# Kernel optimization log

Hardware: AMD Instinct MI355X
Metric: run time of the kernel (lower is better)

Reference implementation:

```python
import jax, jax.numpy as jnp
import numpy as np

MKT_COEF = jnp.array([0.5, -1.0, 0.8, 0.6, 1.5, 0.4], dtype=jnp.float32)
RISK_COEF = jnp.array([0.5, -0.8, 0.6, 1.0, 1.2, 0.5], dtype=jnp.float32)
PI = 3.14159


def setup_inputs() -> dict:
    key = jax.random.key(0)
    k1, k2, k3, k4 = jax.random.split(key, 4)
    B, S, H, D = 128, 8192, 16, 6
    return {
        "sequence_embeddings": jax.random.normal(k1, (B, S, H), dtype=jnp.float32),
        "market_volatility": jax.random.uniform(k2, (B, S), dtype=jnp.float32),
        "risk_factors": jax.random.normal(k3, (B, S, D), dtype=jnp.float32),
        "router_w": jax.random.normal(k4, (D, H), dtype=jnp.float32) * 0.02,
        "router_b": jnp.zeros((D,), dtype=jnp.float32),
    }


def _expert_predictions(x, assignments):
    # x: (B,S,H); assignments: (B,S) int32
    mean = x.mean(-1, keepdims=True)                       # (B,S,1)
    std = jnp.std(x, axis=-1, keepdims=True, ddof=1)       # torch.std is unbiased
    d0 = jnp.tanh(x[:, :, :4].mean(-1, keepdims=True)) * (1.0 + std)
    d1 = jax.nn.sigmoid(mean) * 0.3 - 0.15
    d2 = x[:, :, :6].mean(-1, keepdims=True) * 0.8 + jnp.sin(x[:, :, 6:10].mean(-1, keepdims=True) * PI) * 0.4
    noise = jax.random.normal(jax.random.key(42), mean.shape, dtype=x.dtype) * 0.05
    d3 = jnp.tanh(x[:, :, :8].mean(-1, keepdims=True)) * 0.9 + noise
    d4 = jax.nn.relu(mean) ** 1.2 + std * 2.5 - 0.5
    d5 = jax.nn.sigmoid(mean) * 0.4 + jnp.tanh(std) * 0.2
    preds_all = jnp.concatenate([d0, d1, d2, d3, d4, d5], axis=-1)  # (B,S,6)
    return jnp.take_along_axis(preds_all, assignments[..., None].astype(jnp.int32), axis=-1)  # (B,S,1)


def reference(sequence_embeddings, market_volatility, risk_factors, router_w, router_b):
    x = sequence_embeddings
    logits = jnp.einsum("bsh,dh->bsd", x, router_w) + router_b            # (B,S,6)
    probs_base = jax.nn.softmax(logits, axis=-1)
    assignments = jnp.argmax(probs_base, axis=-1).astype(jnp.int32)       # (B,S)
    # training-mode market/risk adjusted straight-through probs
    adj = logits + market_volatility[..., None] * MKT_COEF * 0.3 + risk_factors * RISK_COEF * 0.3
    probs_diff = jax.nn.softmax(adj / 1.2, axis=-1)
    routing_probs = jax.lax.stop_gradient(probs_base) + probs_diff - jax.lax.stop_gradient(probs_diff)
    predictions = _expert_predictions(x, assignments)                     # (B,S,1)
    return predictions, routing_probs, assignments
```

## Files before the change

kernel.cpp:

```cpp
#include <hip/hip_runtime.h>
#include <math.h>

typedef float float4v __attribute__((ext_vector_type(4)));
typedef float float2v __attribute__((ext_vector_type(2)));

__device__ __forceinline__ unsigned rotl32(unsigned v, int n) {
  return (v << n) | (v >> (32 - n));
}

__device__ __forceinline__ float frcp(float x) { return __builtin_amdgcn_rcpf(x); }

__device__ __forceinline__ float ftanh(float x) {
  float t = __expf(2.0f * x);
  return 1.0f - 2.0f * frcp(t + 1.0f);
}

__device__ __forceinline__ float fsigmoid(float x) {
  return frcp(1.0f + __expf(-x));
}

__device__ __forceinline__ float jax_threefry_normal42_part(unsigned idx) {
  const unsigned ks0 = 0u;
  const unsigned ks1 = 42u;
  const unsigned ks2 = 0x1BD11BDAu ^ 42u;
  unsigned x0 = 0u + ks0;
  unsigned x1 = idx + ks1;
  const unsigned ks[3] = {ks0, ks1, ks2};
  const int rA[4] = {13, 15, 26, 6};
  const int rB[4] = {17, 29, 16, 24};
#pragma unroll
  for (int i = 0; i < 5; ++i) {
    const int* r = (i & 1) ? rB : rA;
#pragma unroll
    for (int k = 0; k < 4; ++k) {
      x0 += x1;
      x1 = rotl32(x1, r[k]);
      x1 ^= x0;
    }
    x0 += ks[(i + 1) % 3];
    x1 += ks[(i + 2) % 3] + (unsigned)(i + 1);
  }
  unsigned bits = x0 ^ x1;
  float u01 = __uint_as_float((bits >> 9) | 0x3f800000u) - 1.0f;
  const float lo = -0.99999994f;
  float u = fmaxf(lo, fmaf(u01, 2.0f, lo));
  float w = -__logf(1.0f - u * u);
  float p;
  if (w < 5.0f) {
    w = w - 2.5f;
    p = 2.81022636e-08f;
    p = fmaf(p, w, 3.43273939e-07f);
    p = fmaf(p, w, -3.5233877e-06f);
    p = fmaf(p, w, -4.39150654e-06f);
    p = fmaf(p, w, 0.00021858087f);
    p = fmaf(p, w, -0.00125372503f);
    p = fmaf(p, w, -0.00417768164f);
    p = fmaf(p, w, 0.246640727f);
    p = fmaf(p, w, 1.50140941f);
  } else {
    w = sqrtf(w) - 3.0f;
    p = -0.000200214257f;
    p = fmaf(p, w, 0.000100950558f);
    p = fmaf(p, w, 0.00134934322f);
    p = fmaf(p, w, -0.00367342844f);
    p = fmaf(p, w, 0.00573950773f);
    p = fmaf(p, w, -0.0076224613f);
    p = fmaf(p, w, 0.00943887047f);
    p = fmaf(p, w, 1.00167406f);
    p = fmaf(p, w, 2.83297682f);
  }
  return 1.41421354f * (p * u);
}

__device__ __forceinline__ void token_body(
    const float4v a[4], int t, float noise,
    const float* __restrict__ rw, const float* __restrict__ rb,
    float* __restrict__ out, int ntok) {
  float2v x2[8];
  x2[0] = a[0].xy; x2[1] = a[0].zw;
  x2[2] = a[1].xy; x2[3] = a[1].zw;
  x2[4] = a[2].xy; x2[5] = a[2].zw;
  x2[6] = a[3].xy; x2[7] = a[3].zw;
  float x[16];
#pragma unroll
  for (int q = 0; q < 4; ++q) {
    x[q * 4 + 0] = a[q].x; x[q * 4 + 1] = a[q].y;
    x[q * 4 + 2] = a[q].z; x[q * 4 + 3] = a[q].w;
  }

  const float2v* rw2 = reinterpret_cast<const float2v*>(rw);
  float lg[6];
#pragma unroll
  for (int d = 0; d < 6; ++d) {
    float2v acc2; acc2.x = 0.0f; acc2.y = 0.0f;
#pragma unroll
    for (int p = 0; p < 8; ++p)
      acc2 = __builtin_elementwise_fma(x2[p], rw2[d * 8 + p], acc2);
    lg[d] = (acc2.x + acc2.y) + rb[d];
  }

  int a1i = 0, a2i = 0;
  float b1 = lg[0], b2 = -1e30f;
#pragma unroll
  for (int d = 1; d < 6; ++d) {
    if (lg[d] > b1) { b2 = b1; a2i = a1i; b1 = lg[d]; a1i = d; }
    else if (lg[d] > b2) { b2 = lg[d]; a2i = d; }
  }
  int amax = a1i;
  if (b1 - b2 < 2e-5f) {
    double A = 0.0, B = 0.0;
#pragma unroll
    for (int h = 0; h < 16; ++h) {
      A = fma((double)x[h], (double)rw[a1i * 16 + h], A);
      B = fma((double)x[h], (double)rw[a2i * 16 + h], B);
    }
    A += (double)rb[a1i];
    B += (double)rb[a2i];
    amax = (B > A || (B == A && a2i < a1i)) ? a2i : a1i;
  }

  float m = lg[0];
#pragma unroll
  for (int d = 1; d < 6; ++d) m = fmaxf(m, lg[d]);
  float eb[6], se = 0.0f;
#pragma unroll
  for (int d = 0; d < 6; ++d) { eb[d] = __expf(lg[d] - m); se += eb[d]; }
  float inv_se = frcp(se);
  float pb[6];
#pragma unroll
  for (int d = 0; d < 6; ++d) pb[d] = eb[d] * inv_se;

  float2v s2; s2.x = 0.0f; s2.y = 0.0f;
#pragma unroll
  for (int p = 0; p < 8; ++p) s2 = s2 + x2[p];
  float mean = (s2.x + s2.y) * (1.0f / 16.0f);
  float2v mean2; mean2.x = mean; mean2.y = mean;
  float2v ss2; ss2.x = 0.0f; ss2.y = 0.0f;
#pragma unroll
  for (int p = 0; p < 8; ++p) {
    float2v dv = x2[p] - mean2;
    ss2 = __builtin_elementwise_fma(dv, dv, ss2);
  }
  float stdv = sqrtf((ss2.x + ss2.y) * (1.0f / 15.0f));

  float s4 = ((x[0] + x[1]) + x[2]) + x[3];
  float s6 = ((((x[0] + x[1]) + x[2]) + x[3]) + x[4]) + x[5];
  float s610 = ((x[6] + x[7]) + x[8]) + x[9];
  float s8 = s6 + x[6] + x[7];

  float sig = fsigmoid(mean);
  float p0 = ftanh(s4 * 0.25f) * (1.0f + stdv);
  float p1 = sig * 0.3f - 0.15f;
  float p2 = (s6 * (1.0f / 6.0f)) * 0.8f + __sinf((s610 * 0.25f) * 3.14159f) * 0.4f;
  float p3 = ftanh(s8 * 0.125f) * 0.9f + noise;
  float r4 = fmaxf(mean, 0.0f);
  float p4 = __expf(1.2f * __logf(r4)) + stdv * 2.5f - 0.5f;
  float p5 = sig * 0.4f + ftanh(stdv) * 0.2f;

  float pred = (amax == 0) ? p0
             : (amax == 1) ? p1
             : (amax == 2) ? p2
             : (amax == 3) ? p3
             : (amax == 4) ? p4
                           : p5;

  out[t] = pred;
  float2v* po = reinterpret_cast<float2v*>(out + ntok) + (size_t)t * 3;
  float2v v0; v0.x = pb[0]; v0.y = pb[1];
  float2v v1; v1.x = pb[2]; v1.y = pb[3];
  float2v v2; v2.x = pb[4]; v2.y = pb[5];
  po[0] = v0;
  po[1] = v1;
  po[2] = v2;
  out[(size_t)ntok * 7 + t] = (float)amax;
}

__global__ __launch_bounds__(256) void finance_moe_kernel(
    const float* __restrict__ emb,
    const float* __restrict__ rw,
    const float* __restrict__ rb,
    float* __restrict__ out,
    int ntok) {
  __shared__ float lds[256 * 16];

  int tl = threadIdx.x;
  int t = blockIdx.x * 256 + tl;
  bool full = ((blockIdx.x + 1) * 256 <= ntok);

  if (full) {
    int lane = tl & 63;
    int wave = tl >> 6;
    const float* gbase = emb + (size_t)blockIdx.x * 256 * 16;
#pragma unroll
    for (int c = 0; c < 4; ++c) {
      int chunk = wave * 4 + c;
      int slot = chunk * 64 + lane;
      int tok = slot >> 2;
      int s = slot & 3;
      int e = s ^ ((tok >> 1) & 3);
      int gidx = tok * 4 + e;
      const float* gp = gbase + (size_t)gidx * 4;
      __builtin_amdgcn_global_load_lds(
          (const __attribute__((address_space(1))) void*)gp,
          (__attribute__((address_space(3))) void*)(lds + (size_t)chunk * 256),
          16, 0, 0);
    }

    float noise = jax_threefry_normal42_part((unsigned)t) * 0.05f;

    __syncthreads();

    float4v a[4];
#pragma unroll
    for (int q = 0; q < 4; ++q) {
      int s = q ^ ((tl >> 1) & 3);
      a[q] = *reinterpret_cast<const float4v*>(&lds[tl * 16 + s * 4]);
    }

    token_body(a, t, noise, rw, rb, out, ntok);
  } else {
    if (t >= ntok) return;
    const float4v* e4 = reinterpret_cast<const float4v*>(emb) + (size_t)t * 4;
    float4v a[4];
    a[0] = e4[0]; a[1] = e4[1]; a[2] = e4[2]; a[3] = e4[3];
    float noise = jax_threefry_normal42_part((unsigned)t) * 0.05f;
    token_body(a, t, noise, rw, rb, out, ntok);
  }
}

extern "C" void kernel_launch(void* const* d_in, const int* in_sizes, int n_in,
                              void* d_out, int out_size, void* d_ws, size_t ws_size,
                              hipStream_t stream) {
  const float* emb = (const float*)d_in[0];
  const float* rw = (const float*)d_in[3];
  const float* rb = (const float*)d_in[4];
  float* out = (float*)d_out;
  int ntok = in_sizes[0] / 16;
  int block = 256;
  int grid = (ntok + block - 1) / block;
  hipLaunchKernelGGL(finance_moe_kernel, dim3(grid), dim3(block), 0, stream,
                     emb, rw, rb, out, ntok);
}
```

Before: 21.86 us.

## Stage routing-prob stores through LDS and load embeddings directly from global

```diff
diff --git a/kernel.cpp b/kernel.cpp
--- a/kernel.cpp
+++ b/kernel.cpp
@@ -72,10 +72,10 @@
   return 1.41421354f * (p * u);
 }
 
-__device__ __forceinline__ void token_body(
-    const float4v a[4], int t, float noise,
+__device__ __forceinline__ void token_compute(
+    const float4v a[4], float noise,
     const float* __restrict__ rw, const float* __restrict__ rb,
-    float* __restrict__ out, int ntok) {
+    float& pred, float* pb, float& asn) {
   float2v x2[8];
   x2[0] = a[0].xy; x2[1] = a[0].zw;
   x2[2] = a[1].xy; x2[3] = a[1].zw;
@@ -126,7 +126,6 @@
 #pragma unroll
   for (int d = 0; d < 6; ++d) { eb[d] = __expf(lg[d] - m); se += eb[d]; }
   float inv_se = frcp(se);
-  float pb[6];
 #pragma unroll
   for (int d = 0; d < 6; ++d) pb[d] = eb[d] * inv_se;
 
@@ -157,22 +156,13 @@
   float p4 = __expf(1.2f * __logf(r4)) + stdv * 2.5f - 0.5f;
   float p5 = sig * 0.4f + ftanh(stdv) * 0.2f;
 
-  float pred = (amax == 0) ? p0
-             : (amax == 1) ? p1
-             : (amax == 2) ? p2
-             : (amax == 3) ? p3
-             : (amax == 4) ? p4
-                           : p5;
-
-  out[t] = pred;
-  float2v* po = reinterpret_cast<float2v*>(out + ntok) + (size_t)t * 3;
-  float2v v0; v0.x = pb[0]; v0.y = pb[1];
-  float2v v1; v1.x = pb[2]; v1.y = pb[3];
-  float2v v2; v2.x = pb[4]; v2.y = pb[5];
-  po[0] = v0;
-  po[1] = v1;
-  po[2] = v2;
-  out[(size_t)ntok * 7 + t] = (float)amax;
+  pred = (amax == 0) ? p0
+       : (amax == 1) ? p1
+       : (amax == 2) ? p2
+       : (amax == 3) ? p3
+       : (amax == 4) ? p4
+                     : p5;
+  asn = (float)amax;
 }
 
 __global__ __launch_bounds__(256) void finance_moe_kernel(
@@ -181,50 +171,42 @@
     const float* __restrict__ rb,
     float* __restrict__ out,
     int ntok) {
-  __shared__ float lds[256 * 16];
+  __shared__ float sprob[256 * 6];
 
   int tl = threadIdx.x;
   int t = blockIdx.x * 256 + tl;
   bool full = ((blockIdx.x + 1) * 256 <= ntok);
 
-  if (full) {
-    int lane = tl & 63;
-    int wave = tl >> 6;
-    const float* gbase = emb + (size_t)blockIdx.x * 256 * 16;
-#pragma unroll
-    for (int c = 0; c < 4; ++c) {
-      int chunk = wave * 4 + c;
-      int slot = chunk * 64 + lane;
-      int tok = slot >> 2;
-      int s = slot & 3;
-      int e = s ^ ((tok >> 1) & 3);
-      int gidx = tok * 4 + e;
-      const float* gp = gbase + (size_t)gidx * 4;
-      __builtin_amdgcn_global_load_lds(
-          (const __attribute__((address_space(1))) void*)gp,
-          (__attribute__((address_space(3))) void*)(lds + (size_t)chunk * 256),
-          16, 0, 0);
-    }
-
-    float noise = jax_threefry_normal42_part((unsigned)t) * 0.05f;
-
-    __syncthreads();
-
-    float4v a[4];
-#pragma unroll
-    for (int q = 0; q < 4; ++q) {
-      int s = q ^ ((tl >> 1) & 3);
-      a[q] = *reinterpret_cast<const float4v*>(&lds[tl * 16 + s * 4]);
-    }
-
-    token_body(a, t, noise, rw, rb, out, ntok);
-  } else {
-    if (t >= ntok) return;
+  float pred = 0.0f, asn = 0.0f;
+  float pb[6];
+  if (t < ntok) {
     const float4v* e4 = reinterpret_cast<const float4v*>(emb) + (size_t)t * 4;
     float4v a[4];
     a[0] = e4[0]; a[1] = e4[1]; a[2] = e4[2]; a[3] = e4[3];
     float noise = jax_threefry_normal42_part((unsigned)t) * 0.05f;
-    token_body(a, t, noise, rw, rb, out, ntok);
+    token_compute(a, noise, rw, rb, pred, pb, asn);
+  }
+
+  if (full) {
+    out[t] = pred;
+    out[(size_t)ntok * 7 + t] = asn;
+#pragma unroll
+    for (int d = 0; d < 6; ++d) sprob[tl * 6 + d] = pb[d];
+    __syncthreads();
+    const float4v* sp4 = reinterpret_cast<const float4v*>(sprob);
+    float4v* pr4 = reinterpret_cast<float4v*>(out + ntok) + (size_t)blockIdx.x * 384;
+    pr4[tl] = sp4[tl];
+    if (tl < 128) pr4[256 + tl] = sp4[256 + tl];
+  } else if (t < ntok) {
+    out[t] = pred;
+    float2v* po = reinterpret_cast<float2v*>(out + ntok) + (size_t)t * 3;
+    float2v v0; v0.x = pb[0]; v0.y = pb[1];
+    float2v v1; v1.x = pb[2]; v1.y = pb[3];
+    float2v v2; v2.x = pb[4]; v2.y = pb[5];
+    po[0] = v0;
+    po[1] = v1;
+    po[2] = v2;
+    out[(size_t)ntok * 7 + t] = asn;
   }
 }
 
```

New measurement: 21.71 us. No clear change (-0.7%).
